# Kernel tuning notes

Hardware: AMD Instinct MI355X
Metric: run time of the kernel (lower is better)

## Reference

```python
import jax, jax.numpy as jnp
import numpy as np

N = 131072
H = 64
CMB_RADIUS_KM = 3485.0


def setup_inputs() -> dict:
    key = jax.random.key(0)
    ks = jax.random.split(key, 8)
    phi = jax.random.uniform(ks[0], (N, 1), jnp.float32, 0.0, 2.0 * np.pi)
    # keep theta away from the poles so sin(theta) != 0
    theta = jax.random.uniform(ks[1], (N, 1), jnp.float32, 0.1, np.pi - 0.1)
    radius = jnp.full((N, 1), CMB_RADIUS_KM, dtype=jnp.float32)
    horiz_theta = jax.random.normal(ks[2], (N, 1), jnp.float32) * 0.01
    horiz_phi = jax.random.normal(ks[3], (N, 1), jnp.float32) * 0.01
    br = jax.random.normal(ks[4], (N, 1), jnp.float32) * 100.0
    W1 = jax.random.normal(ks[5], (2, H), jnp.float32) / np.sqrt(2.0)
    b1 = jnp.zeros((H,), jnp.float32)
    W2 = jax.random.normal(ks[6], (H, H), jnp.float32) / np.sqrt(H)
    b2 = jnp.zeros((H,), jnp.float32)
    W3 = jax.random.normal(ks[7], (H, 1), jnp.float32) / np.sqrt(H)
    b3 = jnp.zeros((1,), jnp.float32)
    return dict(phi=phi, theta=theta, radius=radius, horiz_theta=horiz_theta,
                horiz_phi=horiz_phi, br=br, W1=W1, b1=b1, W2=W2, b2=b2, W3=W3, b3=b3)


def reference(phi, theta, radius, horiz_theta, horiz_phi, br, W1, b1, W2, b2, W3, b3):
    sin = jnp.sin

    # per-point scalar network; input order matches torch.cat([phi, theta], dim=1)
    def T(p, t):
        x = jnp.stack([p, t])
        h = jnp.tanh(x @ W1 + b1)
        h = jnp.tanh(h @ W2 + b2)
        return (h @ W3 + b3)[0]

    dTp = jax.grad(T, 0)
    dTt = jax.grad(T, 1)

    # In the torch code T = model(X) and P = model(X) are the same function,
    # so T_x == P_x and the flows simplify to:
    def u_th(p, t):
        return dTp(p, t) / sin(t) + dTt(p, t)

    def u_ph(p, t):
        return dTp(p, t) / sin(t) - dTt(p, t)

    # nested derivatives exactly as the chained autograd.grad calls
    u_th_t = jax.grad(lambda p, t: -u_th(p, t) * sin(t), 1)            # u_theta_theta
    u_th_tt = jax.grad(lambda p, t: u_th_t(p, t) * sin(t), 1)          # u_theta_theta_theta
    u_th_p = jax.grad(lambda p, t: -u_th(p, t), 0)                     # u_theta_phi
    u_th_pp = jax.grad(u_th_p, 0)                                      # u_theta_phi_phi
    u_ph_t = jax.grad(lambda p, t: u_ph(p, t) * sin(t), 1)             # u_phi_theta
    u_ph_tt = jax.grad(lambda p, t: u_ph_t(p, t) * sin(t), 1)          # u_phi_theta_theta
    u_ph_p = jax.grad(u_ph, 0)                                         # u_phi_phi
    u_ph_pp = jax.grad(u_ph_p, 0)                                      # u_phi_phi_phi

    def per_point(p, t):
        return (u_th(p, t), u_ph(p, t), u_th_t(p, t), u_th_tt(p, t),
                u_th_pp(p, t), u_ph_tt(p, t), u_ph_p(p, t), u_ph_pp(p, t))

    vals = jax.vmap(per_point)(phi.ravel(), theta.ravel())
    ut, up, utt, uttt, utpp, uphtt, upp, uppp = [v.reshape(-1, 1) for v in vals]

    s = sin(theta)
    div_uh = (utt + upp) / (radius * s)
    u_theta_lap = s / radius ** 2 * uttt + utpp / (radius * s) ** 2
    u_phi_lap = s / radius ** 2 * uphtt + uppp / (radius * s) ** 2
    comp = s * (u_theta_lap ** 2 + u_phi_lap ** 2)
    sv_out = -(ut * horiz_theta + up * horiz_phi) - br * div_uh
    tg_con = div_uh - ut * jnp.tan(theta) / radius
    return (ut, up, div_uh, sv_out, tg_con, comp)
```

## Files before the change

kernel.cpp:

```cpp
#include <hip/hip_runtime.h>

#define NH 64

typedef _Float16 half8 __attribute__((ext_vector_type(8)));
typedef float float4v __attribute__((ext_vector_type(4)));

__device__ __forceinline__ float fast_tanh(float x) {
  float ax = fabsf(x);
  float e  = __expf(-2.0f * ax);
  float y  = (1.0f - e) * __builtin_amdgcn_rcpf(1.0f + e);
  return copysignf(y, x);
}

__global__ void prep_B(const float* __restrict__ W2, _Float16* __restrict__ ws) {
  int i = blockIdx.x * 256 + threadIdx.x;
  if (i >= 2 * 4096) return;
  int s = i >> 12;
  int off = i & 4095;
  int nt = off >> 10;
  int ks = (off >> 9) & 1;
  int ln = (off >> 3) & 63;
  int jj = off & 7;
  int h = ks * 32 + (ln >> 4) * 8 + jj;
  int j = nt * 16 + (ln & 15);
  float w2 = W2[h * NH + j];
  _Float16 hi = (_Float16)w2;
  ws[(s * 8 + nt * 2 + ks) * 512 + ln * 8 + jj] =
      (s == 0) ? hi : (_Float16)(w2 - (float)hi);
}

__device__ __forceinline__ half8 ldB(const _Float16* ws, int s, int nt, int ks, int lane) {
  return *(const half8*)(ws + (s * 8 + nt * 2 + ks) * 512 + lane * 8);
}

__global__ __launch_bounds__(256) __attribute__((amdgpu_waves_per_eu(2, 2)))
void pinn_mfma(
    const float* __restrict__ phi, const float* __restrict__ theta,
    const float* __restrict__ radius, const float* __restrict__ hth,
    const float* __restrict__ hph, const float* __restrict__ br,
    const float* __restrict__ W1, const float* __restrict__ b1,
    const float* __restrict__ b2, const float* __restrict__ W3,
    const _Float16* __restrict__ Bws, float* __restrict__ out, int n) {
  const int lane = threadIdx.x & 63;
  const int wave = threadIdx.x >> 6;
  const int tile = blockIdx.x * 4 + wave;
  const int quad = lane >> 4, col = lane & 15;
  const int pbase = tile * 16;
  if (pbase >= n) return;

  float p = phi[pbase + col], t = theta[pbase + col];
  half8 A0h[2], A0l[2], A1h[2], A1l[2], A2h[2], A2l[2];
  half8 A3[2], A4[2], A5[2], A6[2], A7[2], A8[2], A9[2];
#pragma unroll
  for (int ks = 0; ks < 2; ++ks) {
#pragma unroll
    for (int jj = 0; jj < 8; ++jj) {
      int h = ks * 32 + quad * 8 + jj;
      float a = W1[h], b = W1[NH + h];
      float z = fmaf(p, a, fmaf(t, b, b1[h]));
      float y = fast_tanh(z);
      float f1 = fmaf(-y, y, 1.0f);
      float f3 = f1 * fmaf(-6.0f, f1, 4.0f);
      float na = -2.0f * (y * f1);
      float a2 = a * a, ab = a * b, bb = b * b;
      float f3a2 = f3 * a2, f3bb = f3 * bb;
      float v1 = f1 * a, v2 = f1 * b;
      _Float16 yh = (_Float16)y;
      _Float16 v1h = (_Float16)v1;
      _Float16 v2h = (_Float16)v2;
      A0h[ks][jj] = yh;   A0l[ks][jj] = (_Float16)(y - (float)yh);
      A1h[ks][jj] = v1h;  A1l[ks][jj] = (_Float16)(v1 - (float)v1h);
      A2h[ks][jj] = v2h;  A2l[ks][jj] = (_Float16)(v2 - (float)v2h);
      A3[ks][jj] = (_Float16)(na * a2);
      A4[ks][jj] = (_Float16)(na * ab);
      A5[ks][jj] = (_Float16)(na * bb);
      A6[ks][jj] = (_Float16)(f3a2 * a);
      A7[ks][jj] = (_Float16)(f3a2 * b);
      A8[ks][jj] = (_Float16)(f3bb * a);
      A9[ks][jj] = (_Float16)(f3bb * b);
    }
  }

  float4v Tacc[9];
#pragma unroll
  for (int x = 0; x < 9; ++x) Tacc[x] = (float4v){0.f, 0.f, 0.f, 0.f};

#pragma unroll
  for (int nt = 0; nt < 4; ++nt) {
    float4v acc[10];
#pragma unroll
    for (int k = 0; k < 10; ++k) acc[k] = (float4v){0.f, 0.f, 0.f, 0.f};
#pragma unroll
    for (int ks = 0; ks < 2; ++ks) {
      half8 bh = ldB(Bws, 0, nt, ks, lane);
      half8 bl = ldB(Bws, 1, nt, ks, lane);
      acc[0] = __builtin_amdgcn_mfma_f32_16x16x32_f16(A0h[ks], bh, acc[0], 0, 0, 0);
      acc[0] = __builtin_amdgcn_mfma_f32_16x16x32_f16(A0l[ks], bh, acc[0], 0, 0, 0);
      acc[0] = __builtin_amdgcn_mfma_f32_16x16x32_f16(A0h[ks], bl, acc[0], 0, 0, 0);
      acc[1] = __builtin_amdgcn_mfma_f32_16x16x32_f16(A1h[ks], bh, acc[1], 0, 0, 0);
      acc[1] = __builtin_amdgcn_mfma_f32_16x16x32_f16(A1l[ks], bh, acc[1], 0, 0, 0);
      acc[1] = __builtin_amdgcn_mfma_f32_16x16x32_f16(A1h[ks], bl, acc[1], 0, 0, 0);
      acc[2] = __builtin_amdgcn_mfma_f32_16x16x32_f16(A2h[ks], bh, acc[2], 0, 0, 0);
      acc[2] = __builtin_amdgcn_mfma_f32_16x16x32_f16(A2l[ks], bh, acc[2], 0, 0, 0);
      acc[2] = __builtin_amdgcn_mfma_f32_16x16x32_f16(A2h[ks], bl, acc[2], 0, 0, 0);
      acc[3] = __builtin_amdgcn_mfma_f32_16x16x32_f16(A3[ks], bh, acc[3], 0, 0, 0);
      acc[4] = __builtin_amdgcn_mfma_f32_16x16x32_f16(A4[ks], bh, acc[4], 0, 0, 0);
      acc[5] = __builtin_amdgcn_mfma_f32_16x16x32_f16(A5[ks], bh, acc[5], 0, 0, 0);
      acc[6] = __builtin_amdgcn_mfma_f32_16x16x32_f16(A6[ks], bh, acc[6], 0, 0, 0);
      acc[7] = __builtin_amdgcn_mfma_f32_16x16x32_f16(A7[ks], bh, acc[7], 0, 0, 0);
      acc[8] = __builtin_amdgcn_mfma_f32_16x16x32_f16(A8[ks], bh, acc[8], 0, 0, 0);
      acc[9] = __builtin_amdgcn_mfma_f32_16x16x32_f16(A9[ks], bh, acc[9], 0, 0, 0);
    }
    float b2v = b2[nt * 16 + col];
    float w3v = W3[nt * 16 + col];
#pragma unroll
    for (int r = 0; r < 4; ++r) {
      float z0 = acc[0][r] + b2v;
      float y2 = fast_tanh(z0);
      float g1 = fmaf(-y2, y2, 1.0f);
      float g2 = -2.0f * (y2 * g1);
      float g3 = g1 * fmaf(-6.0f, g1, 4.0f);
      float gp = acc[1][r], gt = acc[2][r];
      float gpp = acc[3][r], gpt = acc[4][r], gtt = acc[5][r];
      float zppp = acc[6][r], zppt = acc[7][r], zptt = acc[8][r], zttt = acc[9][r];
      float gp2 = gp * gp, gt2 = gt * gt;
      Tacc[0][r] = fmaf(w3v, g1 * gp, Tacc[0][r]);
      Tacc[1][r] = fmaf(w3v, g1 * gt, Tacc[1][r]);
      Tacc[2][r] = fmaf(w3v, fmaf(g2, gp2, g1 * gpp), Tacc[2][r]);
      Tacc[3][r] = fmaf(w3v, fmaf(g2, gp * gt, g1 * gpt), Tacc[3][r]);
      Tacc[4][r] = fmaf(w3v, fmaf(g2, gt2, g1 * gtt), Tacc[4][r]);
      Tacc[5][r] = fmaf(w3v, fmaf(g3, gp2 * gp, fmaf(3.0f * g2, gp * gpp, g1 * zppp)), Tacc[5][r]);
      Tacc[6][r] = fmaf(w3v, fmaf(g3, gp2 * gt, fmaf(g2, fmaf(2.0f, gp * gpt, gt * gpp), g1 * zppt)), Tacc[6][r]);
      Tacc[7][r] = fmaf(w3v, fmaf(g3, gp * gt2, fmaf(g2, fmaf(2.0f, gt * gpt, gp * gtt), g1 * zptt)), Tacc[7][r]);
      Tacc[8][r] = fmaf(w3v, fmaf(g3, gt2 * gt, fmaf(3.0f * g2, gt * gtt, g1 * zttt)), Tacc[8][r]);
    }
  }

  float T[9];
#pragma unroll
  for (int x = 0; x < 9; ++x) {
    float4v v = Tacc[x];
    bool hi8 = (col & 8) != 0;
    float k0 = hi8 ? v[2] : v[0];
    float k1 = hi8 ? v[3] : v[1];
    float s0 = hi8 ? v[0] : v[2];
    float s1 = hi8 ? v[1] : v[3];
    float p0 = k0 + __shfl_xor(s0, 8, 16);
    float p1 = k1 + __shfl_xor(s1, 8, 16);
    bool hi4 = (col & 4) != 0;
    float kk = hi4 ? p1 : p0;
    float ss = hi4 ? p0 : p1;
    float q = kk + __shfl_xor(ss, 4, 16);
    q += __shfl_xor(q, 2, 16);
    q += __shfl_xor(q, 1, 16);
    T[x] = q;
  }
  float Tp = T[0], Tt = T[1], Tpp = T[2], Tpt = T[3], Ttt = T[4];
  float Tppp = T[5], Tppt = T[6], Tptt = T[7], Tttt = T[8];

  int rsel = col >> 2;
  int pi = pbase + quad * 4 + rsel;
  float t2 = theta[pi];
  float s, c;
  __sincosf(t2, &s, &c);
  float inv_s = __builtin_amdgcn_rcpf(s);
  float inv_s2 = inv_s * inv_s;

  float A = Tp * inv_s + Tt;
  float D = Tp * inv_s - Tt;
  float q1 = Tpt * inv_s - Tp * c * inv_s2;
  float A_t = q1 + Ttt;
  float D_t = q1 - Ttt;
  float q2 = Tptt * inv_s - 2.0f * Tpt * c * inv_s2
           + Tp * (s * s + 2.0f * c * c) * inv_s2 * inv_s;
  float A_tt = q2 + Tttt;
  float D_tt = q2 - Tttt;
  float A_pp = Tppp * inv_s + Tppt;
  float D_p  = Tpp * inv_s - Tpt;
  float D_pp = Tppp * inv_s - Tppt;

  float utt   = -(A_t * s + A * c);
  float uttt  = -(A_tt * s + 2.0f * A_t * c - A * s) * s + utt * c;
  float utpp  = -A_pp;
  float upht  = D_t * s + D * c;
  float uphtt = (D_tt * s + 2.0f * D_t * c - D * s) * s + upht * c;
  float upp   = D_p;
  float uppp  = D_pp;

  float r = radius[pi];
  float inv_r = __builtin_amdgcn_rcpf(r);
  float inv_r2 = inv_r * inv_r;
  float div_uh = (utt + upp) * inv_r * inv_s;
  float lap_t = s * inv_r2 * uttt + utpp * inv_s2 * inv_r2;
  float lap_p = s * inv_r2 * uphtt + uppp * inv_s2 * inv_r2;
  float comp = s * (lap_t * lap_t + lap_p * lap_p);
  float sv = -(A * hth[pi] + D * hph[pi]) - br[pi] * div_uh;
  float tg = div_uh - A * s * __builtin_amdgcn_rcpf(c) * inv_r;

  if ((col & 3) == 0) {
    out[pi]         = A;
    out[n + pi]     = D;
    out[2 * n + pi] = div_uh;
    out[3 * n + pi] = sv;
    out[4 * n + pi] = tg;
    out[5 * n + pi] = comp;
  }
}

extern "C" void kernel_launch(void* const* d_in, const int* in_sizes, int n_in,
                              void* d_out, int out_size, void* d_ws, size_t ws_size,
                              hipStream_t stream) {
  const float* phi    = (const float*)d_in[0];
  const float* theta  = (const float*)d_in[1];
  const float* radius = (const float*)d_in[2];
  const float* hth    = (const float*)d_in[3];
  const float* hph    = (const float*)d_in[4];
  const float* br     = (const float*)d_in[5];
  const float* W1     = (const float*)d_in[6];
  const float* b1     = (const float*)d_in[7];
  const float* W2     = (const float*)d_in[8];
  const float* b2     = (const float*)d_in[9];
  const float* W3     = (const float*)d_in[10];
  (void)ws_size; (void)n_in; (void)out_size;

  _Float16* Bws = (_Float16*)d_ws;
  float* out = (float*)d_out;
  int n = in_sizes[0];

  prep_B<<<(2 * 4096 + 255) / 256, 256, 0, stream>>>(W2, Bws);
  int ntiles = (n + 15) / 16;
  int nblocks = (ntiles + 3) / 4;
  pinn_mfma<<<nblocks, 256, 0, stream>>>(
      phi, theta, radius, hth, hph, br, W1, b1, b2, W3, Bws, out, n);
}
```

Measured before the change: 110.3 us.

## Fuse W2 fp16 split into main kernel via LDS and hoist per-point loads

```diff
diff --git a/kernel.cpp b/kernel.cpp
--- a/kernel.cpp
+++ b/kernel.cpp
@@ -6,31 +6,9 @@
 typedef float float4v __attribute__((ext_vector_type(4)));
 
 __device__ __forceinline__ float fast_tanh(float x) {
-  float ax = fabsf(x);
-  float e  = __expf(-2.0f * ax);
-  float y  = (1.0f - e) * __builtin_amdgcn_rcpf(1.0f + e);
-  return copysignf(y, x);
-}
-
-__global__ void prep_B(const float* __restrict__ W2, _Float16* __restrict__ ws) {
-  int i = blockIdx.x * 256 + threadIdx.x;
-  if (i >= 2 * 4096) return;
-  int s = i >> 12;
-  int off = i & 4095;
-  int nt = off >> 10;
-  int ks = (off >> 9) & 1;
-  int ln = (off >> 3) & 63;
-  int jj = off & 7;
-  int h = ks * 32 + (ln >> 4) * 8 + jj;
-  int j = nt * 16 + (ln & 15);
-  float w2 = W2[h * NH + j];
-  _Float16 hi = (_Float16)w2;
-  ws[(s * 8 + nt * 2 + ks) * 512 + ln * 8 + jj] =
-      (s == 0) ? hi : (_Float16)(w2 - (float)hi);
-}
-
-__device__ __forceinline__ half8 ldB(const _Float16* ws, int s, int nt, int ks, int lane) {
-  return *(const half8*)(ws + (s * 8 + nt * 2 + ks) * 512 + lane * 8);
+  float e = __expf(2.0f * x);
+  float r = __builtin_amdgcn_rcpf(e + 1.0f);
+  return fmaf(-2.0f, r, 1.0f);
 }
 
 __global__ __launch_bounds__(256) __attribute__((amdgpu_waves_per_eu(2, 2)))
@@ -39,8 +17,21 @@
     const float* __restrict__ radius, const float* __restrict__ hth,
     const float* __restrict__ hph, const float* __restrict__ br,
     const float* __restrict__ W1, const float* __restrict__ b1,
-    const float* __restrict__ b2, const float* __restrict__ W3,
-    const _Float16* __restrict__ Bws, float* __restrict__ out, int n) {
+    const float* __restrict__ W2, const float* __restrict__ b2,
+    const float* __restrict__ W3, float* __restrict__ out, int n) {
+  __shared__ _Float16 Bs[2 * 4096];
+
+  for (int i = threadIdx.x; i < 4096; i += 256) {
+    int h = i >> 6, j = i & 63;
+    float w2 = W2[i];
+    int nt = j >> 4, cl = j & 15, ks = h >> 5, q = (h >> 3) & 3, j2 = h & 7;
+    int base = (nt * 2 + ks) * 512 + (q * 16 + cl) * 8 + j2;
+    _Float16 hi = (_Float16)w2;
+    Bs[base] = hi;
+    Bs[base + 4096] = (_Float16)(w2 - (float)hi);
+  }
+  __syncthreads();
+
   const int lane = threadIdx.x & 63;
   const int wave = threadIdx.x >> 6;
   const int tile = blockIdx.x * 4 + wave;
@@ -81,6 +72,18 @@
     }
   }
 
+  const int rsel = col >> 2;
+  const int pi = pbase + quad * 4 + rsel;
+  float t2 = theta[pi];
+  float rv = radius[pi];
+  float hthv = hth[pi], hphv = hph[pi], brv = br[pi];
+  float b2a[4], w3a[4];
+#pragma unroll
+  for (int nt = 0; nt < 4; ++nt) {
+    b2a[nt] = b2[nt * 16 + col];
+    w3a[nt] = W3[nt * 16 + col];
+  }
+
   float4v Tacc[9];
 #pragma unroll
   for (int x = 0; x < 9; ++x) Tacc[x] = (float4v){0.f, 0.f, 0.f, 0.f};
@@ -92,8 +95,8 @@
     for (int k = 0; k < 10; ++k) acc[k] = (float4v){0.f, 0.f, 0.f, 0.f};
 #pragma unroll
     for (int ks = 0; ks < 2; ++ks) {
-      half8 bh = ldB(Bws, 0, nt, ks, lane);
-      half8 bl = ldB(Bws, 1, nt, ks, lane);
+      half8 bh = *(const half8*)(Bs + (nt * 2 + ks) * 512 + lane * 8);
+      half8 bl = *(const half8*)(Bs + 4096 + (nt * 2 + ks) * 512 + lane * 8);
       acc[0] = __builtin_amdgcn_mfma_f32_16x16x32_f16(A0h[ks], bh, acc[0], 0, 0, 0);
       acc[0] = __builtin_amdgcn_mfma_f32_16x16x32_f16(A0l[ks], bh, acc[0], 0, 0, 0);
       acc[0] = __builtin_amdgcn_mfma_f32_16x16x32_f16(A0h[ks], bl, acc[0], 0, 0, 0);
@@ -111,8 +114,8 @@
       acc[8] = __builtin_amdgcn_mfma_f32_16x16x32_f16(A8[ks], bh, acc[8], 0, 0, 0);
       acc[9] = __builtin_amdgcn_mfma_f32_16x16x32_f16(A9[ks], bh, acc[9], 0, 0, 0);
     }
-    float b2v = b2[nt * 16 + col];
-    float w3v = W3[nt * 16 + col];
+    float b2v = b2a[nt];
+    float w3v = w3a[nt];
 #pragma unroll
     for (int r = 0; r < 4; ++r) {
       float z0 = acc[0][r] + b2v;
@@ -123,16 +126,18 @@
       float gp = acc[1][r], gt = acc[2][r];
       float gpp = acc[3][r], gpt = acc[4][r], gtt = acc[5][r];
       float zppp = acc[6][r], zppt = acc[7][r], zptt = acc[8][r], zttt = acc[9][r];
+      float c2p = g2 * gp, c2t = g2 * gt;
+      float c2p2 = c2p + c2p, c2t2 = c2t + c2t;
       float gp2 = gp * gp, gt2 = gt * gt;
       Tacc[0][r] = fmaf(w3v, g1 * gp, Tacc[0][r]);
       Tacc[1][r] = fmaf(w3v, g1 * gt, Tacc[1][r]);
-      Tacc[2][r] = fmaf(w3v, fmaf(g2, gp2, g1 * gpp), Tacc[2][r]);
-      Tacc[3][r] = fmaf(w3v, fmaf(g2, gp * gt, g1 * gpt), Tacc[3][r]);
-      Tacc[4][r] = fmaf(w3v, fmaf(g2, gt2, g1 * gtt), Tacc[4][r]);
-      Tacc[5][r] = fmaf(w3v, fmaf(g3, gp2 * gp, fmaf(3.0f * g2, gp * gpp, g1 * zppp)), Tacc[5][r]);
-      Tacc[6][r] = fmaf(w3v, fmaf(g3, gp2 * gt, fmaf(g2, fmaf(2.0f, gp * gpt, gt * gpp), g1 * zppt)), Tacc[6][r]);
-      Tacc[7][r] = fmaf(w3v, fmaf(g3, gp * gt2, fmaf(g2, fmaf(2.0f, gt * gpt, gp * gtt), g1 * zptt)), Tacc[7][r]);
-      Tacc[8][r] = fmaf(w3v, fmaf(g3, gt2 * gt, fmaf(3.0f * g2, gt * gtt, g1 * zttt)), Tacc[8][r]);
+      Tacc[2][r] = fmaf(w3v, fmaf(c2p, gp, g1 * gpp), Tacc[2][r]);
+      Tacc[3][r] = fmaf(w3v, fmaf(c2p, gt, g1 * gpt), Tacc[3][r]);
+      Tacc[4][r] = fmaf(w3v, fmaf(c2t, gt, g1 * gtt), Tacc[4][r]);
+      Tacc[5][r] = fmaf(w3v, fmaf(g3, gp2 * gp, fmaf(c2p2 + c2p, gpp, g1 * zppp)), Tacc[5][r]);
+      Tacc[6][r] = fmaf(w3v, fmaf(g3, gp2 * gt, fmaf(c2p2, gpt, fmaf(c2t, gpp, g1 * zppt))), Tacc[6][r]);
+      Tacc[7][r] = fmaf(w3v, fmaf(g3, gp * gt2, fmaf(c2t2, gpt, fmaf(c2p, gtt, g1 * zptt))), Tacc[7][r]);
+      Tacc[8][r] = fmaf(w3v, fmaf(g3, gt2 * gt, fmaf(c2t2 + c2t, gtt, g1 * zttt)), Tacc[8][r]);
     }
   }
 
@@ -158,11 +163,9 @@
   float Tp = T[0], Tt = T[1], Tpp = T[2], Tpt = T[3], Ttt = T[4];
   float Tppp = T[5], Tppt = T[6], Tptt = T[7], Tttt = T[8];
 
-  int rsel = col >> 2;
-  int pi = pbase + quad * 4 + rsel;
-  float t2 = theta[pi];
-  float s, c;
-  __sincosf(t2, &s, &c);
+  float rev = t2 * 0.15915494309189535f;
+  float s = __builtin_amdgcn_sinf(rev);
+  float c = __builtin_amdgcn_cosf(rev);
   float inv_s = __builtin_amdgcn_rcpf(s);
   float inv_s2 = inv_s * inv_s;
 
@@ -187,14 +190,13 @@
   float upp   = D_p;
   float uppp  = D_pp;
 
-  float r = radius[pi];
-  float inv_r = __builtin_amdgcn_rcpf(r);
+  float inv_r = __builtin_amdgcn_rcpf(rv);
   float inv_r2 = inv_r * inv_r;
   float div_uh = (utt + upp) * inv_r * inv_s;
   float lap_t = s * inv_r2 * uttt + utpp * inv_s2 * inv_r2;
   float lap_p = s * inv_r2 * uphtt + uppp * inv_s2 * inv_r2;
   float comp = s * (lap_t * lap_t + lap_p * lap_p);
-  float sv = -(A * hth[pi] + D * hph[pi]) - br[pi] * div_uh;
+  float sv = -(A * hthv + D * hphv) - brv * div_uh;
   float tg = div_uh - A * s * __builtin_amdgcn_rcpf(c) * inv_r;
 
   if ((col & 3) == 0) {
@@ -221,15 +223,13 @@
   const float* W2     = (const float*)d_in[8];
   const float* b2     = (const float*)d_in[9];
   const float* W3     = (const float*)d_in[10];
-  (void)ws_size; (void)n_in; (void)out_size;
-
-  _Float16* Bws = (_Float16*)d_ws;
+  (void)ws_size; (void)n_in; (void)out_size; (void)d_ws;
+
   float* out = (float*)d_out;
   int n = in_sizes[0];
 
-  prep_B<<<(2 * 4096 + 255) / 256, 256, 0, stream>>>(W2, Bws);
   int ntiles = (n + 15) / 16;
   int nblocks = (ntiles + 3) / 4;
   pinn_mfma<<<nblocks, 256, 0, stream>>>(
-      phi, theta, radius, hth, hph, br, W1, b1, b2, W3, Bws, out, n);
+      phi, theta, radius, hth, hph, br, W1, b1, W2, b2, W3, out, n);
 }
```

Result: no change. 111.8 us (+1.3%).
